# Performance work log

Measured on AMD Instinct MI355X. Metric: run time of the kernel, lower is better.

The kernel has to match this reference:

```python
import jax, jax.numpy as jnp
import numpy as np

N, E = 100000, 1600000
NODE_IN, EDGE_IN, H = 128, 16, 128


def sage_conv(x, src, dst, Wl, Wr, b, n_nodes):
    # PyG SAGEConv (aggr='mean'): out = lin_l(mean_{j->i} x_j) + lin_r(x_i), bias on lin_l
    msg_sum = jax.ops.segment_sum(x[src], dst, num_segments=n_nodes)      # [N, d]
    cnt = jax.ops.segment_sum(jnp.ones((src.shape[0],), x.dtype), dst, num_segments=n_nodes)
    mean = msg_sum / jnp.maximum(cnt, 1.0)[:, None]                        # empty neighborhoods -> 0
    return mean @ Wl + x @ Wr + b


def setup_inputs() -> dict:
    key = jax.random.key(0)
    ks = jax.random.split(key, 12)
    s = lambda d: 1.0 / np.sqrt(d)
    return {
        "x": jax.random.normal(ks[0], (N, NODE_IN), jnp.float32),
        "edge_index": jax.random.randint(ks[1], (2, E), 0, N, dtype=jnp.int64),
        "edge_attr": jax.random.normal(ks[2], (E, EDGE_IN), jnp.float32),
        "Wl1": jax.random.normal(ks[3], (NODE_IN, H), jnp.float32) * s(NODE_IN),
        "Wr1": jax.random.normal(ks[4], (NODE_IN, H), jnp.float32) * s(NODE_IN),
        "b1": jnp.zeros((H,), jnp.float32),
        "Wl2": jax.random.normal(ks[5], (H, H), jnp.float32) * s(H),
        "Wr2": jax.random.normal(ks[6], (H, H), jnp.float32) * s(H),
        "b2": jnp.zeros((H,), jnp.float32),
        "Wm1": jax.random.normal(ks[7], (2 * H + EDGE_IN, H), jnp.float32) * s(2 * H + EDGE_IN),
        "bm1": jnp.zeros((H,), jnp.float32),
        "Wm2": jax.random.normal(ks[8], (H, 1), jnp.float32) * s(H),
        "bm2": jnp.zeros((1,), jnp.float32),
    }


def reference(x, edge_index, edge_attr, Wl1, Wr1, b1, Wl2, Wr2, b2, Wm1, bm1, Wm2, bm2):
    src, dst = edge_index[0], edge_index[1]
    h = jax.nn.relu(sage_conv(x, src, dst, Wl1, Wr1, b1, N))
    h = jax.nn.relu(sage_conv(h, src, dst, Wl2, Wr2, b2, N))
    edge_feat = jnp.concatenate([h[src], h[dst], edge_attr], axis=1)  # [E, 2H+edge_in]
    out = jax.nn.relu(edge_feat @ Wm1 + bm1) @ Wm2 + bm2               # dropout is identity in eval
    return out.reshape(-1)
```

## Files before the change

### kernel.cpp

```cpp
#include <hip/hip_runtime.h>

typedef _Float16 f16;
typedef _Float16 f16x2 __attribute__((ext_vector_type(2)));
typedef _Float16 f16x8 __attribute__((ext_vector_type(8)));
typedef float f32x4 __attribute__((ext_vector_type(4)));

#define MFMA16(a,b,c) __builtin_amdgcn_mfma_f32_16x16x32_f16((a),(b),(c),0,0,0)

__global__ void k_detect(const long long* ei, int n_nodes, int* flag) {
    long long v = ei[threadIdx.x];
    int bad = (v < 0 || v >= n_nodes);
    unsigned long long m = __ballot(bad);
    if (threadIdx.x == 0) *flag = (m == 0ULL);
}

__global__ void k_idx(const void* ei, int E, const int* __restrict__ flag,
                      int* __restrict__ src, int* __restrict__ dst,
                      int* __restrict__ deg) {
    int e = blockIdx.x * 256 + threadIdx.x;
    if (e >= E) return;
    int s, d;
    if (*flag) {
        const long long* p = (const long long*)ei;
        s = (int)p[e];
        d = (int)p[(size_t)E + e];
    } else {
        const int* p = (const int*)ei;
        s = p[e];
        d = p[(size_t)E + e];
    }
    src[e] = s;
    dst[e] = d;
    atomicAdd(&deg[d], 1);
}

__device__ __forceinline__ void wfrag_body(const float* Wa, const float* Wb,
                                           f16* dst, int t) {
    int l = t & 63;
    int s = t >> 9;
    int k0 = s * 32 + (l >> 4) * 8;
    int j = ((t >> 6) & 7) * 16 + (l & 15);
    f16x8 h;
    #pragma unroll
    for (int e = 0; e < 8; e++) {
        int k = k0 + e;
        float v = (k < 128) ? Wa[k * 128 + j] : Wb[(k - 128) * 128 + j];
        h[e] = (f16)v;
    }
    *(f16x8*)(dst + (size_t)t * 8) = h;
}

__global__ void k_prep(const float* __restrict__ x,
                       const float* __restrict__ Wl1, const float* __restrict__ Wr1,
                       const float* __restrict__ Wl2, const float* __restrict__ Wr2,
                       const float* __restrict__ Wm1,
                       f16* __restrict__ xh, f16* __restrict__ w1f, f16* __restrict__ w2f,
                       f16* __restrict__ zwf, f16* __restrict__ wef, int N) {
    const int xb = (N * 16 + 255) / 256;
    int b = blockIdx.x;
    if (b < xb) {
        int i = (b * 256 + threadIdx.x) * 8;
        if (i >= N * 128) return;
        float4 a = *(const float4*)(x + i);
        float4 c = *(const float4*)(x + i + 4);
        f16x8 h;
        h[0] = (f16)a.x; h[1] = (f16)a.y; h[2] = (f16)a.z; h[3] = (f16)a.w;
        h[4] = (f16)c.x; h[5] = (f16)c.y; h[6] = (f16)c.z; h[7] = (f16)c.w;
        *(f16x8*)(xh + i) = h;
        return;
    }
    b -= xb;
    if (b < 16) { wfrag_body(Wl1, Wr1, w1f, b * 256 + threadIdx.x); return; }
    if (b < 32) { wfrag_body(Wl2, Wr2, w2f, (b - 16) * 256 + threadIdx.x); return; }
    if (b < 48) {
        int t = (b - 32) * 256 + threadIdx.x;
        int lane = t & 63, c = (t >> 6) & 15, s = t >> 10;
        int k0 = s * 32 + (lane >> 4) * 8;
        int j = c * 16 + (lane & 15);
        f16x8 h;
        #pragma unroll
        for (int e = 0; e < 8; e++) {
            int k = k0 + e;
            float v = (j < 128) ? Wm1[k * 128 + j] : Wm1[(128 + k) * 128 + (j - 128)];
            h[e] = (f16)v;
        }
        *(f16x8*)(zwf + (size_t)t * 8) = h;
        return;
    }
    {
        int t = (b - 48) * 256 + threadIdx.x;
        if (t >= 8 * 64) return;
        int lane = t & 63, ct = t >> 6;
        int k0 = (lane >> 4) * 8;
        int j = (ct >> 1) * 32 + 2 * (lane & 15) + (ct & 1);
        f16x8 h;
        #pragma unroll
        for (int e = 0; e < 8; e++) {
            int k = k0 + e;
            h[e] = (k < 16) ? (f16)Wm1[(256 + k) * 128 + j] : (f16)0.0f;
        }
        *(f16x8*)(wef + (size_t)t * 8) = h;
    }
}

__global__ void k_bsum(const int* __restrict__ deg, int n, int* __restrict__ bsum) {
    __shared__ int ws[4];
    const int tid = threadIdx.x;
    int i = blockIdx.x * 1024 + tid * 4;
    int s = 0;
    if (i + 3 < n) {
        int4 d = *(const int4*)(deg + i);
        s = d.x + d.y + d.z + d.w;
    } else {
        #pragma unroll
        for (int j = 0; j < 4; j++) if (i + j < n) s += deg[i + j];
    }
    #pragma unroll
    for (int m = 1; m < 64; m <<= 1) s += __shfl_xor(s, m, 64);
    if ((tid & 63) == 0) ws[tid >> 6] = s;
    __syncthreads();
    if (tid == 0) bsum[blockIdx.x] = ws[0] + ws[1] + ws[2] + ws[3];
}

__global__ void k_bscan(int* __restrict__ bsum, int nb, int* __restrict__ rowptr_n) {
    __shared__ int wsum[4];
    const int tid = threadIdx.x, lane = tid & 63, wid = tid >> 6;
    int v = (tid < nb) ? bsum[tid] : 0;
    int inc = v;
    #pragma unroll
    for (int off = 1; off < 64; off <<= 1) {
        int u = __shfl_up(inc, off, 64);
        if (lane >= off) inc += u;
    }
    if (lane == 63) wsum[wid] = inc;
    __syncthreads();
    int woff = 0;
    for (int j = 0; j < wid; j++) woff += wsum[j];
    int excl = woff + inc - v;
    if (tid < nb) bsum[tid] = excl;
    if (tid == nb - 1) rowptr_n[0] = excl + v;
}

__global__ void k_rowptr(const int* __restrict__ deg, int n, const int* __restrict__ boff,
                         int* __restrict__ rowptr, int* __restrict__ cursor) {
    __shared__ int wsum[4];
    const int tid = threadIdx.x, lane = tid & 63, wid = tid >> 6;
    int i = blockIdx.x * 1024 + tid * 4;
    int d0 = 0, d1 = 0, d2 = 0, d3 = 0;
    if (i + 3 < n) {
        int4 d = *(const int4*)(deg + i);
        d0 = d.x; d1 = d.y; d2 = d.z; d3 = d.w;
    } else {
        if (i     < n) d0 = deg[i];
        if (i + 1 < n) d1 = deg[i + 1];
        if (i + 2 < n) d2 = deg[i + 2];
        if (i + 3 < n) d3 = deg[i + 3];
    }
    int s = d0 + d1 + d2 + d3;
    int inc = s;
    #pragma unroll
    for (int off = 1; off < 64; off <<= 1) {
        int u = __shfl_up(inc, off, 64);
        if (lane >= off) inc += u;
    }
    if (lane == 63) wsum[wid] = inc;
    __syncthreads();
    int woff = 0;
    for (int j = 0; j < wid; j++) woff += wsum[j];
    int excl = boff[blockIdx.x] + woff + inc - s;
    int e1 = excl + d0, e2 = e1 + d1, e3 = e2 + d2;
    if (i     < n) { rowptr[i]     = excl; cursor[i]     = excl; }
    if (i + 1 < n) { rowptr[i + 1] = e1;   cursor[i + 1] = e1; }
    if (i + 2 < n) { rowptr[i + 2] = e2;   cursor[i + 2] = e2; }
    if (i + 3 < n) { rowptr[i + 3] = e3;   cursor[i + 3] = e3; }
}

__global__ void k_scatter(const int* __restrict__ src, const int* __restrict__ dst, int E,
                          int* __restrict__ cursor, int* __restrict__ col,
                          int4* __restrict__ pk, int* __restrict__ pos) {
    int e = blockIdx.x * 256 + threadIdx.x;
    if (e < E) {
        int s = src[e], d = dst[e];
        int p = atomicAdd(&cursor[d], 1);
        col[p] = s;
        pk[p] = make_int4(s, e, d, 0);
        pos[e] = p;
    }
}

#define AP 136
template<int DO_Z>
__global__ __launch_bounds__(256, DO_Z ? 4 : 5) void k_fuse(
    const f16* __restrict__ tab,
    const int* __restrict__ rowptr, const int* __restrict__ col,
    const f16* __restrict__ Wf, const float* __restrict__ bias,
    const f16* __restrict__ zwf, const float* __restrict__ bm1,
    f16* __restrict__ out, int n_rows) {
    __shared__ __align__(16) f16 sA[64 * AP];
    const int tid = threadIdx.x, lane = tid & 63, w = tid >> 6;
    const int l15 = lane & 15, g = lane >> 4;
    const int base = blockIdx.x * 64;

    const int g16 = tid >> 4, c = tid & 15;
    #pragma unroll
    for (int rep = 0; rep < 4; rep++) {
        const int node = base + rep * 16 + g16;
        float acc[8] = {0.f, 0.f, 0.f, 0.f, 0.f, 0.f, 0.f, 0.f};
        int d = 1;
        if (node < n_rows) {
            const int s0 = rowptr[node], s1 = rowptr[node + 1];
            int k = s0;
            for (; k + 3 < s1; k += 4) {
                const int n0 = col[k], n1 = col[k + 1], n2 = col[k + 2], n3 = col[k + 3];
                f16x8 v0 = *(const f16x8*)(tab + (size_t)n0 * 128 + c * 8);
                f16x8 v1 = *(const f16x8*)(tab + (size_t)n1 * 128 + c * 8);
                f16x8 v2 = *(const f16x8*)(tab + (size_t)n2 * 128 + c * 8);
                f16x8 v3 = *(const f16x8*)(tab + (size_t)n3 * 128 + c * 8);
                #pragma unroll
                for (int j = 0; j < 8; j++)
                    acc[j] += ((float)v0[j] + (float)v1[j]) + ((float)v2[j] + (float)v3[j]);
            }
            for (; k < s1; ++k) {
                const int n0 = col[k];
                f16x8 v0 = *(const f16x8*)(tab + (size_t)n0 * 128 + c * 8);
                #pragma unroll
                for (int j = 0; j < 8; j++) acc[j] += (float)v0[j];
            }
            d = s1 - s0; if (d < 1) d = 1;
        }
        const float inv = 1.f / (float)d;
        f16x8 r;
        #pragma unroll
        for (int j = 0; j < 8; j++) r[j] = (f16)(acc[j] * inv);
        *(f16x8*)&sA[(rep * 16 + g16) * AP + c * 8] = r;
    }
    __syncthreads();

    const int c0 = (2 * w) * 16 + l15, c1 = c0 + 16;
    const float b0 = bias[c0], b1 = bias[c1];
    f32x4 acc[4][2];
    #pragma unroll
    for (int t = 0; t < 4; t++) {
        acc[t][0] = f32x4{b0, b0, b0, b0};
        acc[t][1] = f32x4{b1, b1, b1, b1};
    }
    #pragma unroll
    for (int s = 0; s < 8; s++) {
        f16x8 bf0 = *(const f16x8*)&Wf[((size_t)(s * 8 + 2 * w    ) * 64 + lane) * 8];
        f16x8 bf1 = *(const f16x8*)&Wf[((size_t)(s * 8 + 2 * w + 1) * 64 + lane) * 8];
        const int koff = (s & 3) * 32 + g * 8;
        #pragma unroll
        for (int t = 0; t < 4; t++) {
            f16x8 a;
            if (s < 4) {
                a = *(const f16x8*)&sA[(t * 16 + l15) * AP + koff];
            } else {
                int row = base + t * 16 + l15;
                if (row >= n_rows) row = n_rows - 1;
                a = *(const f16x8*)(tab + (size_t)row * 128 + koff);
            }
            acc[t][0] = MFMA16(a, bf0, acc[t][0]);
            acc[t][1] = MFMA16(a, bf1, acc[t][1]);
        }
    }

    if (DO_Z == 0) {
        #pragma unroll
        for (int t = 0; t < 4; t++) {
            #pragma unroll
            for (int i = 0; i < 4; i++) {
                int row = base + t * 16 + g * 4 + i;
                if (row < n_rows) {
                    float v0 = acc[t][0][i]; v0 = v0 > 0.f ? v0 : 0.f;
                    float v1 = acc[t][1][i]; v1 = v1 > 0.f ? v1 : 0.f;
                    out[(size_t)row * 128 + c0] = (f16)v0;
                    out[(size_t)row * 128 + c1] = (f16)v1;
                }
            }
        }
    } else {
        __syncthreads();
        #pragma unroll
        for (int t = 0; t < 4; t++) {
            #pragma unroll
            for (int i = 0; i < 4; i++) {
                const int rl = t * 16 + g * 4 + i;
                float v0 = acc[t][0][i]; v0 = v0 > 0.f ? v0 : 0.f;
                float v1 = acc[t][1][i]; v1 = v1 > 0.f ? v1 : 0.f;
                sA[rl * AP + c0] = (f16)v0;
                sA[rl * AP + c1] = (f16)v1;
            }
        }
        __syncthreads();
        #pragma unroll
        for (int half = 0; half < 2; half++) {
            const int j0 = (4 * w + 2 * half) * 16 + l15, j1 = j0 + 16;
            const float zb0 = (j0 >= 128) ? bm1[j0 - 128] : 0.0f;
            const float zb1 = (j1 >= 128) ? bm1[j1 - 128] : 0.0f;
            f32x4 zacc[4][2];
            #pragma unroll
            for (int t = 0; t < 4; t++) {
                zacc[t][0] = f32x4{zb0, zb0, zb0, zb0};
                zacc[t][1] = f32x4{zb1, zb1, zb1, zb1};
            }
            #pragma unroll
            for (int s = 0; s < 4; s++) {
                f16x8 wf0 = *(const f16x8*)&zwf[((size_t)(s * 16 + 4 * w + 2 * half    ) * 64 + lane) * 8];
                f16x8 wf1 = *(const f16x8*)&zwf[((size_t)(s * 16 + 4 * w + 2 * half + 1) * 64 + lane) * 8];
                const int koff = s * 32 + g * 8;
                #pragma unroll
                for (int t = 0; t < 4; t++) {
                    f16x8 a = *(const f16x8*)&sA[(t * 16 + l15) * AP + koff];
                    zacc[t][0] = MFMA16(a, wf0, zacc[t][0]);
                    zacc[t][1] = MFMA16(a, wf1, zacc[t][1]);
                }
            }
            #pragma unroll
            for (int t = 0; t < 4; t++) {
                #pragma unroll
                for (int i = 0; i < 4; i++) {
                    int row = base + t * 16 + g * 4 + i;
                    if (row < n_rows) {
                        out[(size_t)row * 256 + j0] = (f16)zacc[t][0][i];
                        out[(size_t)row * 256 + j1] = (f16)zacc[t][1][i];
                    }
                }
            }
        }
    }
}

#define ZP3 136
__global__ __launch_bounds__(256, 4) void k_edge3(
    const f16* __restrict__ z, const float* __restrict__ ea,
    const int4* __restrict__ pk,
    const f16* __restrict__ wef, const float* __restrict__ Wm2,
    const float* __restrict__ bm2, float* __restrict__ tmp,
    int E, int iters, int nwaves) {
    __shared__ __align__(16) f16 sZ[4][16 * ZP3];
    const int tid = threadIdx.x, lane = tid & 63, w = tid >> 6;
    const int l15 = lane & 15, g = lane >> 4;
    const int te = lane >> 2, sq = lane & 3;
    const int gw = blockIdx.x * 4 + w;

    f16x8 be[8];
    #pragma unroll
    for (int cc = 0; cc < 8; cc++)
        be[cc] = *(const f16x8*)(wef + ((size_t)(cc * 64 + lane)) * 8);
    float2 w2p[4];
    #pragma unroll
    for (int pg = 0; pg < 4; pg++)
        w2p[pg] = *(const float2*)&Wm2[pg * 32 + 2 * l15];
    const float bv = bm2[0];

    f16* myZ = &sZ[w][0];

    f16x8 zs[4], zd[4];
    f16x8 a_cur, a_next;

    auto stage_load = [&](int pbase, f16x8* zsv, f16x8* zdv, f16x8& av) {
        int pr = pbase + te; if (pr > E - 1) pr = E - 1;
        const int4 v = pk[pr];
        const int is = v.x, id = v.z;
        const f16* ps = z + (size_t)is * 256 + sq * 8;
        const f16* pd = z + (size_t)id * 256 + 128 + sq * 8;
        #pragma unroll
        for (int i = 0; i < 4; i++) {
            zsv[i] = *(const f16x8*)(ps + i * 32);
            zdv[i] = *(const f16x8*)(pd + i * 32);
        }
        int pe = pbase + l15; if (pe > E - 1) pe = E - 1;
        f16x8 av_ = {};
        if (g < 2) {
            const int ee2 = pk[pe].y;
            float4 e0 = *(const float4*)(ea + (size_t)ee2 * 16 + g * 8);
            float4 e1 = *(const float4*)(ea + (size_t)ee2 * 16 + g * 8 + 4);
            av_[0] = (f16)e0.x; av_[1] = (f16)e0.y; av_[2] = (f16)e0.z; av_[3] = (f16)e0.w;
            av_[4] = (f16)e1.x; av_[5] = (f16)e1.y; av_[6] = (f16)e1.z; av_[7] = (f16)e1.w;
        }
        av = av_;
    };
    auto stage_write = [&]() {
        f16* zp = myZ + te * ZP3 + sq * 8;
        #pragma unroll
        for (int i = 0; i < 4; i++) {
            f16x8 v = zs[i] + zd[i];
            *(f16x8*)(zp + i * 32) = v;
        }
    };

    stage_load(gw * 16, zs, zd, a_cur);
    stage_write();

    for (int it = 0; it < iters; ++it) {
        const int pbase = (gw + it * nwaves) * 16;
        if (pbase >= E) break;
        const int nxt = (gw + (it + 1) * nwaves) * 16;
        const bool has_next = (it + 1 < iters) && (nxt < E);
        if (has_next) stage_load(nxt, zs, zd, a_next);

        f32x4 acc[8];
        #pragma unroll
        for (int cc = 0; cc < 8; cc++) acc[cc] = f32x4{0.f, 0.f, 0.f, 0.f};
        #pragma unroll
        for (int cc = 0; cc < 8; cc++) acc[cc] = MFMA16(a_cur, be[cc], acc[cc]);

        float p[4];
        #pragma unroll
        for (int i = 0; i < 4; i++) {
            const int edge = g * 4 + i;
            float s = 0.f;
            #pragma unroll
            for (int pg = 0; pg < 4; pg++) {
                f16x2 zz = *(const f16x2*)&myZ[edge * ZP3 + pg * 32 + 2 * l15];
                float v0 = (float)zz[0] + acc[2 * pg    ][i]; v0 = v0 > 0.f ? v0 : 0.f;
                float v1 = (float)zz[1] + acc[2 * pg + 1][i]; v1 = v1 > 0.f ? v1 : 0.f;
                s += v0 * w2p[pg].x + v1 * w2p[pg].y;
            }
            p[i] = s;
        }
        #pragma unroll
        for (int m = 1; m < 16; m <<= 1)
            #pragma unroll
            for (int i = 0; i < 4; i++) p[i] += __shfl_xor(p[i], m, 64);
        if (l15 == 0) {
            #pragma unroll
            for (int i = 0; i < 4; i++) {
                int pp = pbase + g * 4 + i;
                if (pp < E) tmp[pp] = p[i] + bv;
            }
        }
        if (has_next) {
            stage_write();
            a_cur = a_next;
        }
    }
}

__global__ void k_perm(const float* __restrict__ tmp, const int* __restrict__ pos,
                       float* __restrict__ out, int E) {
    int e = blockIdx.x * 256 + threadIdx.x;
    if (e < E) out[e] = tmp[pos[e]];
}

extern "C" void kernel_launch(void* const* d_in, const int* in_sizes, int n_in,
                              void* d_out, int out_size, void* d_ws, size_t ws_size,
                              hipStream_t stream) {
    const float* x   = (const float*)d_in[0];
    const void*  ei  = d_in[1];
    const float* ea  = (const float*)d_in[2];
    const float* Wl1 = (const float*)d_in[3];
    const float* Wr1 = (const float*)d_in[4];
    const float* b1  = (const float*)d_in[5];
    const float* Wl2 = (const float*)d_in[6];
    const float* Wr2 = (const float*)d_in[7];
    const float* b2  = (const float*)d_in[8];
    const float* Wm1 = (const float*)d_in[9];
    const float* bm1 = (const float*)d_in[10];
    const float* Wm2 = (const float*)d_in[11];
    const float* bm2 = (const float*)d_in[12];

    const int N = in_sizes[0] / 128;
    const int E = in_sizes[1] / 2;

    char* ws = (char*)d_ws;
    size_t off = 0;
    auto alloc = [&](size_t bytes) -> void* {
        void* p = ws + off;
        off = (off + bytes + 255) & ~(size_t)255;
        return p;
    };
    f16* z      = (f16*)alloc((size_t)N * 256 * 2);
    f16* xh     = z;
    f16* h1     = (f16*)alloc((size_t)N * 128 * 2);
    int* src    = (int*)alloc((size_t)E * 4);
    int* dst    = (int*)alloc((size_t)E * 4);
    int* col    = (int*)alloc((size_t)E * 4);
    int4* pk    = (int4*)alloc((size_t)E * 16);
    int* pos    = (int*)alloc((size_t)E * 4);
    float* tmp  = (float*)alloc((size_t)E * 4);
    int* deg    = (int*)alloc((size_t)N * 4);
    int* rowptr = (int*)alloc((size_t)(N + 1) * 4);
    int* cursor = (int*)alloc((size_t)N * 4);
    int* bsum   = (int*)alloc((size_t)1024 * 4);
    f16* w1f    = (f16*)alloc((size_t)8 * 8 * 64 * 8 * 2);
    f16* w2f    = (f16*)alloc((size_t)8 * 8 * 64 * 8 * 2);
    f16* zwf    = (f16*)alloc((size_t)4 * 16 * 64 * 8 * 2);
    f16* wef    = (f16*)alloc((size_t)8 * 64 * 8 * 2);
    int* flag   = (int*)alloc(4);
    if (off > ws_size) return;

    const int eb = (E + 255) / 256;
    const int nbk = (N + 1023) / 1024;
    const int rb64 = (N + 63) / 64;

    k_detect<<<1, 64, 0, stream>>>((const long long*)ei, N, flag);
    hipMemsetAsync(deg, 0, (size_t)N * 4, stream);
    k_idx<<<eb, 256, 0, stream>>>(ei, E, flag, src, dst, deg);
    const int xb = (N * 16 + 255) / 256;
    k_prep<<<xb + 50, 256, 0, stream>>>(x, Wl1, Wr1, Wl2, Wr2, Wm1,
                                        xh, w1f, w2f, zwf, wef, N);

    k_bsum<<<nbk, 256, 0, stream>>>(deg, N, bsum);
    k_bscan<<<1, 256, 0, stream>>>(bsum, nbk, rowptr + N);
    k_rowptr<<<nbk, 256, 0, stream>>>(deg, N, bsum, rowptr, cursor);
    k_scatter<<<eb, 256, 0, stream>>>(src, dst, E, cursor, col, pk, pos);

    k_fuse<0><<<rb64, 256, 0, stream>>>(xh, rowptr, col, w1f, b1, nullptr, nullptr, h1, N);
    k_fuse<1><<<rb64, 256, 0, stream>>>(h1, rowptr, col, w2f, b2, zwf, bm1, z, N);

    const int eg = 1792;
    const int nwaves = eg * 4;
    const int ntiles = (E + 15) / 16;
    const int e_iters = (ntiles + nwaves - 1) / nwaves;
    k_edge3<<<eg, 256, 0, stream>>>(z, ea, pk, wef, Wm2, bm2,
                                    tmp, E, e_iters, nwaves);
    k_perm<<<eb, 256, 0, stream>>>(tmp, pos, (float*)d_out, E);
}
```

Before: 502.8 us.

## Process edges in original order, dropping packed CSR edge array and permutation pass

The edge MLP kernel now walks edges in their original order, reading src/dst and edge_attr directly and writing straight to the output. This removes the packed int4 array, the position array, the temporary output buffer and the final permutation kernel, which cuts scatter writes and one launch. The trade-off is that consecutive edges now gather z rows for random destinations instead of dst-sorted ones, which may lower cache locality on the dst half of the gather.

```diff
diff --git a/kernel.cpp b/kernel.cpp
--- a/kernel.cpp
+++ b/kernel.cpp
@@ -176,15 +176,11 @@
 }
 
 __global__ void k_scatter(const int* __restrict__ src, const int* __restrict__ dst, int E,
-                          int* __restrict__ cursor, int* __restrict__ col,
-                          int4* __restrict__ pk, int* __restrict__ pos) {
+                          int* __restrict__ cursor, int* __restrict__ col) {
     int e = blockIdx.x * 256 + threadIdx.x;
     if (e < E) {
-        int s = src[e], d = dst[e];
-        int p = atomicAdd(&cursor[d], 1);
-        col[p] = s;
-        pk[p] = make_int4(s, e, d, 0);
-        pos[e] = p;
+        int p = atomicAdd(&cursor[dst[e]], 1);
+        col[p] = src[e];
     }
 }
 
@@ -333,9 +329,9 @@
 #define ZP3 136
 __global__ __launch_bounds__(256, 4) void k_edge3(
     const f16* __restrict__ z, const float* __restrict__ ea,
-    const int4* __restrict__ pk,
+    const int* __restrict__ src, const int* __restrict__ dst,
     const f16* __restrict__ wef, const float* __restrict__ Wm2,
-    const float* __restrict__ bm2, float* __restrict__ tmp,
+    const float* __restrict__ bm2, float* __restrict__ out,
     int E, int iters, int nwaves) {
     __shared__ __align__(16) f16 sZ[4][16 * ZP3];
     const int tid = threadIdx.x, lane = tid & 63, w = tid >> 6;
@@ -360,8 +356,7 @@
 
     auto stage_load = [&](int pbase, f16x8* zsv, f16x8* zdv, f16x8& av) {
         int pr = pbase + te; if (pr > E - 1) pr = E - 1;
-        const int4 v = pk[pr];
-        const int is = v.x, id = v.z;
+        const int is = src[pr], id = dst[pr];
         const f16* ps = z + (size_t)is * 256 + sq * 8;
         const f16* pd = z + (size_t)id * 256 + 128 + sq * 8;
         #pragma unroll
@@ -372,9 +367,8 @@
         int pe = pbase + l15; if (pe > E - 1) pe = E - 1;
         f16x8 av_ = {};
         if (g < 2) {
-            const int ee2 = pk[pe].y;
-            float4 e0 = *(const float4*)(ea + (size_t)ee2 * 16 + g * 8);
-            float4 e1 = *(const float4*)(ea + (size_t)ee2 * 16 + g * 8 + 4);
+            float4 e0 = *(const float4*)(ea + (size_t)pe * 16 + g * 8);
+            float4 e1 = *(const float4*)(ea + (size_t)pe * 16 + g * 8 + 4);
             av_[0] = (f16)e0.x; av_[1] = (f16)e0.y; av_[2] = (f16)e0.z; av_[3] = (f16)e0.w;
             av_[4] = (f16)e1.x; av_[5] = (f16)e1.y; av_[6] = (f16)e1.z; av_[7] = (f16)e1.w;
         }
@@ -427,7 +421,7 @@
             #pragma unroll
             for (int i = 0; i < 4; i++) {
                 int pp = pbase + g * 4 + i;
-                if (pp < E) tmp[pp] = p[i] + bv;
+                if (pp < E) out[pp] = p[i] + bv;
             }
         }
         if (has_next) {
@@ -435,12 +429,6 @@
             a_cur = a_next;
         }
     }
-}
-
-__global__ void k_perm(const float* __restrict__ tmp, const int* __restrict__ pos,
-                       float* __restrict__ out, int E) {
-    int e = blockIdx.x * 256 + threadIdx.x;
-    if (e < E) out[e] = tmp[pos[e]];
 }
 
 extern "C" void kernel_launch(void* const* d_in, const int* in_sizes, int n_in,
@@ -476,9 +464,6 @@
     int* src    = (int*)alloc((size_t)E * 4);
     int* dst    = (int*)alloc((size_t)E * 4);
     int* col    = (int*)alloc((size_t)E * 4);
-    int4* pk    = (int4*)alloc((size_t)E * 16);
-    int* pos    = (int*)alloc((size_t)E * 4);
-    float* tmp  = (float*)alloc((size_t)E * 4);
     int* deg    = (int*)alloc((size_t)N * 4);
     int* rowptr = (int*)alloc((size_t)(N + 1) * 4);
     int* cursor = (int*)alloc((size_t)N * 4);
@@ -504,7 +489,7 @@
     k_bsum<<<nbk, 256, 0, stream>>>(deg, N, bsum);
     k_bscan<<<1, 256, 0, stream>>>(bsum, nbk, rowptr + N);
     k_rowptr<<<nbk, 256, 0, stream>>>(deg, N, bsum, rowptr, cursor);
-    k_scatter<<<eb, 256, 0, stream>>>(src, dst, E, cursor, col, pk, pos);
+    k_scatter<<<eb, 256, 0, stream>>>(src, dst, E, cursor, col);
 
     k_fuse<0><<<rb64, 256, 0, stream>>>(xh, rowptr, col, w1f, b1, nullptr, nullptr, h1, N);
     k_fuse<1><<<rb64, 256, 0, stream>>>(h1, rowptr, col, w2f, b2, zwf, bm1, z, N);
@@ -513,7 +498,6 @@
     const int nwaves = eg * 4;
     const int ntiles = (E + 15) / 16;
     const int e_iters = (ntiles + nwaves - 1) / nwaves;
-    k_edge3<<<eg, 256, 0, stream>>>(z, ea, pk, wef, Wm2, bm2,
-                                    tmp, E, e_iters, nwaves);
-    k_perm<<<eb, 256, 0, stream>>>(tmp, pos, (float*)d_out, E);
-}
+    k_edge3<<<eg, 256, 0, stream>>>(z, ea, src, dst, wef, Wm2, bm2,
+                                    (float*)d_out, E, e_iters, nwaves);
+}
```

After: 519.6 us. 1.03x slower.

## Split per-node degree and cursor counters into 8 sub-slots to cut atomic contention

Applied to the files above, without the earlier changes.

Degree counting and CSR scatter now use 8 sub-counters per node, picked by block index, and the prefix scan runs over N*8 entries so each node's edges form 8 contiguous sub-segments. The aim is to spread same-address atomics across more locations. In exchange the scan arrays grow eightfold, the block-scan kernel runs with 1024 threads, and the fused kernels read rowptr with a stride of 8. The per-node atomics were not heavily contended at an average degree of 16, so the larger scan may cost more than it saves.

```diff
diff --git a/kernel.cpp b/kernel.cpp
--- a/kernel.cpp
+++ b/kernel.cpp
@@ -16,7 +16,7 @@
 
 __global__ void k_idx(const void* ei, int E, const int* __restrict__ flag,
                       int* __restrict__ src, int* __restrict__ dst,
-                      int* __restrict__ deg) {
+                      int* __restrict__ deg8) {
     int e = blockIdx.x * 256 + threadIdx.x;
     if (e >= E) return;
     int s, d;
@@ -31,7 +31,7 @@
     }
     src[e] = s;
     dst[e] = d;
-    atomicAdd(&deg[d], 1);
+    atomicAdd(&deg8[(size_t)d * 8 + (blockIdx.x & 7)], 1);
 }
 
 __device__ __forceinline__ void wfrag_body(const float* Wa, const float* Wb,
@@ -123,7 +123,7 @@
 }
 
 __global__ void k_bscan(int* __restrict__ bsum, int nb, int* __restrict__ rowptr_n) {
-    __shared__ int wsum[4];
+    __shared__ int wsum[16];
     const int tid = threadIdx.x, lane = tid & 63, wid = tid >> 6;
     int v = (tid < nb) ? bsum[tid] : 0;
     int inc = v;
@@ -134,8 +134,17 @@
     }
     if (lane == 63) wsum[wid] = inc;
     __syncthreads();
-    int woff = 0;
-    for (int j = 0; j < wid; j++) woff += wsum[j];
+    if (tid < 16) {
+        int t = wsum[tid];
+        #pragma unroll
+        for (int off = 1; off < 16; off <<= 1) {
+            int u = __shfl_up(t, off, 64);
+            if (tid >= off) t += u;
+        }
+        wsum[tid] = t;
+    }
+    __syncthreads();
+    int woff = (wid == 0) ? 0 : wsum[wid - 1];
     int excl = woff + inc - v;
     if (tid < nb) bsum[tid] = excl;
     if (tid == nb - 1) rowptr_n[0] = excl + v;
@@ -176,12 +185,12 @@
 }
 
 __global__ void k_scatter(const int* __restrict__ src, const int* __restrict__ dst, int E,
-                          int* __restrict__ cursor, int* __restrict__ col,
+                          int* __restrict__ cursor8, int* __restrict__ col,
                           int4* __restrict__ pk, int* __restrict__ pos) {
     int e = blockIdx.x * 256 + threadIdx.x;
     if (e < E) {
         int s = src[e], d = dst[e];
-        int p = atomicAdd(&cursor[d], 1);
+        int p = atomicAdd(&cursor8[(size_t)d * 8 + (blockIdx.x & 7)], 1);
         col[p] = s;
         pk[p] = make_int4(s, e, d, 0);
         pos[e] = p;
@@ -192,7 +201,7 @@
 template<int DO_Z>
 __global__ __launch_bounds__(256, DO_Z ? 4 : 5) void k_fuse(
     const f16* __restrict__ tab,
-    const int* __restrict__ rowptr, const int* __restrict__ col,
+    const int* __restrict__ rowptr8, const int* __restrict__ col,
     const f16* __restrict__ Wf, const float* __restrict__ bias,
     const f16* __restrict__ zwf, const float* __restrict__ bm1,
     f16* __restrict__ out, int n_rows) {
@@ -208,7 +217,7 @@
         float acc[8] = {0.f, 0.f, 0.f, 0.f, 0.f, 0.f, 0.f, 0.f};
         int d = 1;
         if (node < n_rows) {
-            const int s0 = rowptr[node], s1 = rowptr[node + 1];
+            const int s0 = rowptr8[node * 8], s1 = rowptr8[node * 8 + 8];
             int k = s0;
             for (; k + 3 < s1; k += 4) {
                 const int n0 = col[k], n1 = col[k + 1], n2 = col[k + 2], n3 = col[k + 3];
@@ -462,6 +471,7 @@
 
     const int N = in_sizes[0] / 128;
     const int E = in_sizes[1] / 2;
+    const int NV = N * 8;
 
     char* ws = (char*)d_ws;
     size_t off = 0;
@@ -479,9 +489,9 @@
     int4* pk    = (int4*)alloc((size_t)E * 16);
     int* pos    = (int*)alloc((size_t)E * 4);
     float* tmp  = (float*)alloc((size_t)E * 4);
-    int* deg    = (int*)alloc((size_t)N * 4);
-    int* rowptr = (int*)alloc((size_t)(N + 1) * 4);
-    int* cursor = (int*)alloc((size_t)N * 4);
+    int* deg8   = (int*)alloc((size_t)NV * 4);
+    int* rowptr = (int*)alloc((size_t)(NV + 1) * 4);
+    int* cursor = (int*)alloc((size_t)NV * 4);
     int* bsum   = (int*)alloc((size_t)1024 * 4);
     f16* w1f    = (f16*)alloc((size_t)8 * 8 * 64 * 8 * 2);
     f16* w2f    = (f16*)alloc((size_t)8 * 8 * 64 * 8 * 2);
@@ -491,19 +501,19 @@
     if (off > ws_size) return;
 
     const int eb = (E + 255) / 256;
-    const int nbk = (N + 1023) / 1024;
+    const int nbk8 = (NV + 1023) / 1024;
     const int rb64 = (N + 63) / 64;
 
     k_detect<<<1, 64, 0, stream>>>((const long long*)ei, N, flag);
-    hipMemsetAsync(deg, 0, (size_t)N * 4, stream);
-    k_idx<<<eb, 256, 0, stream>>>(ei, E, flag, src, dst, deg);
+    hipMemsetAsync(deg8, 0, (size_t)NV * 4, stream);
+    k_idx<<<eb, 256, 0, stream>>>(ei, E, flag, src, dst, deg8);
     const int xb = (N * 16 + 255) / 256;
     k_prep<<<xb + 50, 256, 0, stream>>>(x, Wl1, Wr1, Wl2, Wr2, Wm1,
                                         xh, w1f, w2f, zwf, wef, N);
 
-    k_bsum<<<nbk, 256, 0, stream>>>(deg, N, bsum);
-    k_bscan<<<1, 256, 0, stream>>>(bsum, nbk, rowptr + N);
-    k_rowptr<<<nbk, 256, 0, stream>>>(deg, N, bsum, rowptr, cursor);
+    k_bsum<<<nbk8, 256, 0, stream>>>(deg8, NV, bsum);
+    k_bscan<<<1, 1024, 0, stream>>>(bsum, nbk8, rowptr + NV);
+    k_rowptr<<<nbk8, 256, 0, stream>>>(deg8, NV, bsum, rowptr, cursor);
     k_scatter<<<eb, 256, 0, stream>>>(src, dst, E, cursor, col, pk, pos);
 
     k_fuse<0><<<rb64, 256, 0, stream>>>(xh, rowptr, col, w1f, b1, nullptr, nullptr, h1, N);
```

Result: no change. 510.3 us (+1.5%).
